# Optimization experiments

Measured on AMD Instinct MI355X. Metric: run time of the kernel, lower is better.

## Reference

```python
import jax, jax.numpy as jnp
import numpy as np

B, S, H = 64, 1024, 1024

def setup_inputs() -> dict:
    key = jax.random.key(0)
    k1, k2, k3, k4, k5 = jax.random.split(key, 5)
    scale = 1.0 / np.sqrt(H)
    return {
        "decoder_state": jax.random.normal(k1, (B, H), dtype=jnp.float32),
        "encoder_outputs": jax.random.normal(k2, (B, S, H), dtype=jnp.float32),
        "mask": jnp.ones((B, S), dtype=jnp.int32),
        "W_s": jax.random.uniform(k3, (H, H), minval=-scale, maxval=scale, dtype=jnp.float32),
        "W_h": jax.random.uniform(k4, (H, H), minval=-scale, maxval=scale, dtype=jnp.float32),
        "v": jax.random.uniform(k5, (H,), minval=-scale, maxval=scale, dtype=jnp.float32),
    }

def reference(decoder_state, encoder_outputs, mask, W_s, W_h, v):
    # Additive (Bahdanau) attention.
    # proj_s: [B, H] -- original applies W_s to the expanded state (same math, computed once)
    proj_s = decoder_state @ W_s.T
    # proj_h: [B, S, H]
    proj_h = jnp.einsum('bsh,kh->bsk', encoder_outputs, W_h)
    energy = jnp.tanh(proj_s[:, None, :] + proj_h)          # [B, S, H]
    scores = jnp.einsum('bsh,h->bs', energy, v)             # [B, S]
    scores = jnp.where(mask == 0, -jnp.inf, scores)
    weights = jax.nn.softmax(scores, axis=-1)               # [B, S]
    context = jnp.einsum('bs,bsh->bh', weights, encoder_outputs)  # [B, H]
    return context, weights
```

## Files before the change

### kernel.cpp

```cpp
#include <hip/hip_runtime.h>
#include <hip/hip_bf16.h>

#define B_ 64
#define S_ 1024
#define H_ 1024
#define M_ (B_*S_)

typedef __attribute__((ext_vector_type(8))) short short8;
typedef __attribute__((ext_vector_type(4))) float f32x4;

__device__ __forceinline__ unsigned short f2bf(float f) {
    union { float f; unsigned u; } c; c.f = f;
    unsigned u = c.u;
    unsigned r = (u + 0x7fffu + ((u >> 16) & 1u)) >> 16;
    return (unsigned short)r;
}

__device__ __forceinline__ float bf2f(unsigned short h) {
    union { unsigned u; float f; } c; c.u = ((unsigned)h) << 16;
    return c.f;
}

__device__ __forceinline__ float tanh_fast(float x) {
    float t = __expf(2.0f * x);
    return 1.0f - 2.0f * __builtin_amdgcn_rcpf(t + 1.0f);
}

__device__ __forceinline__ void gll16(const unsigned short* g, unsigned short* l) {
    auto* gp = (const __attribute__((address_space(1))) unsigned short*)(g);
    auto* lp = (__attribute__((address_space(3))) unsigned short*)(l);
    __builtin_amdgcn_global_load_lds(gp, lp, 16, 0, 0);
}

__global__ void cvt_bf16_kernel(const float* __restrict__ src,
                                unsigned short* __restrict__ dst, int n8) {
    int idx = blockIdx.x * blockDim.x + threadIdx.x;
    int stride = gridDim.x * blockDim.x;
    for (int i = idx; i < n8; i += stride) {
        const float4* s4 = (const float4*)src + (size_t)i * 2;
        float4 a = s4[0], b = s4[1];
        short8 o;
        o[0] = f2bf(a.x); o[1] = f2bf(a.y); o[2] = f2bf(a.z); o[3] = f2bf(a.w);
        o[4] = f2bf(b.x); o[5] = f2bf(b.y); o[6] = f2bf(b.z); o[7] = f2bf(b.w);
        *((short8*)dst + i) = o;
    }
}

__global__ void proj_s_part_kernel(const float* __restrict__ dec,
                                   const float* __restrict__ Ws,
                                   float* __restrict__ part) {
    __shared__ float wss[64][68];
    const int kt = blockIdx.x & 15, hs = blockIdx.x >> 4;
    const int k0 = kt * 64, h0 = hs * 64;
    const int t = threadIdx.x;

    {
        const int r = t >> 2, c = (t & 3) * 16;
        const float4* src = (const float4*)(Ws + (size_t)(k0 + r) * H_ + h0 + c);
        float4 v0 = src[0], v1 = src[1], v2 = src[2], v3 = src[3];
        *(float4*)&wss[r][c + 0]  = v0;
        *(float4*)&wss[r][c + 4]  = v1;
        *(float4*)&wss[r][c + 8]  = v2;
        *(float4*)&wss[r][c + 12] = v3;
    }
    const int b = t >> 2, kq = t & 3;
    float4 dreg[16];
    const float4* dsrc = (const float4*)(dec + (size_t)b * H_ + h0);
#pragma unroll
    for (int i = 0; i < 16; ++i) dreg[i] = dsrc[i];
    __syncthreads();

    float acc[16] = {};
#pragma unroll
    for (int h4 = 0; h4 < 16; ++h4) {
        float4 d = dreg[h4];
#pragma unroll
        for (int j = 0; j < 16; ++j) {
            float4 wv = *(const float4*)&wss[kq + 4 * j][h4 * 4];
            acc[j] = fmaf(d.x, wv.x, acc[j]);
            acc[j] = fmaf(d.y, wv.y, acc[j]);
            acc[j] = fmaf(d.z, wv.z, acc[j]);
            acc[j] = fmaf(d.w, wv.w, acc[j]);
        }
    }
#pragma unroll
    for (int j = 0; j < 16; ++j)
        part[(size_t)hs * M_ + b * H_ + k0 + kq + 4 * j] = acc[j];
}

__global__ void proj_red_kernel(const float* __restrict__ part,
                                float* __restrict__ proj_s) {
    int i = blockIdx.x * 256 + threadIdx.x;
    float s = 0.0f;
#pragma unroll
    for (int p = 0; p < 16; ++p) s += part[(size_t)p * M_ + i];
    proj_s[i] = s;
}

__global__ void fused_scores_bf16_kernel(const unsigned short* __restrict__ encb,
                                         const unsigned short* __restrict__ Whb,
                                         const float* __restrict__ proj_s,
                                         const float* __restrict__ v,
                                         float* __restrict__ scores_part) {
    __shared__ __align__(16) unsigned short AsF[128 * 32];
    __shared__ __align__(16) unsigned short BsF[128 * 32];
    __shared__ float sums[128][2];

    const int bx0 = blockIdx.x;
    const int bx = (bx0 & 7) * 512 + (bx0 >> 3);
    const int nt = bx & 7;
    const int mt = bx >> 3;
    const int t = threadIdx.x;
    const int w = t >> 6, lane = t & 63;
    const int wr = w >> 1, wc = w & 1;
    const int lrow = lane & 15, lgrp = lane >> 4;

    f32x4 acc[4][4] = {};

    const int srow = lane >> 2;
    const int scol = (lane & 3) * 8;
    const unsigned short* gA0 = encb + (size_t)(mt * 128 + w * 32 + srow) * H_ + scol;
    const unsigned short* gA1 = gA0 + 16 * H_;
    const unsigned short* gB0 = Whb + (size_t)(nt * 128 + w * 32 + srow) * H_ + scol;
    const unsigned short* gB1 = gB0 + 16 * H_;
    unsigned short* lA0 = AsF + (w * 2 + 0) * 512;
    unsigned short* lA1 = AsF + (w * 2 + 1) * 512;
    unsigned short* lB0 = BsF + (w * 2 + 0) * 512;
    unsigned short* lB1 = BsF + (w * 2 + 1) * 512;

    for (int kt = 0; kt < H_ / 32; ++kt) {
        __syncthreads();
        gll16(gA0 + kt * 32, lA0);
        gll16(gA1 + kt * 32, lA1);
        gll16(gB0 + kt * 32, lB0);
        gll16(gB1 + kt * 32, lB1);
        __syncthreads();

        short8 af[4], bf[4];
#pragma unroll
        for (int m = 0; m < 4; ++m)
            af[m] = *(const short8*)&AsF[(wr * 64 + m * 16 + lrow) * 32 + lgrp * 8];
#pragma unroll
        for (int n = 0; n < 4; ++n)
            bf[n] = *(const short8*)&BsF[(wc * 64 + n * 16 + lrow) * 32 + lgrp * 8];
#pragma unroll
        for (int m = 0; m < 4; ++m)
#pragma unroll
            for (int n = 0; n < 4; ++n)
                acc[m][n] = __builtin_amdgcn_mfma_f32_16x16x32_bf16(af[m], bf[n], acc[m][n], 0, 0, 0);
    }

    const int b = mt >> 3;
    float vv[4], ps[4];
#pragma unroll
    for (int n = 0; n < 4; ++n) {
        int col = nt * 128 + wc * 64 + n * 16 + lrow;
        vv[n] = v[col];
        ps[n] = proj_s[b * H_ + col];
    }
    float rs[4][4];
#pragma unroll
    for (int m = 0; m < 4; ++m) {
#pragma unroll
        for (int j = 0; j < 4; ++j) {
            float s = 0.0f;
#pragma unroll
            for (int n = 0; n < 4; ++n)
                s = fmaf(tanh_fast(acc[m][n][j] + ps[n]), vv[n], s);
            s += __shfl_xor(s, 1, 64);
            s += __shfl_xor(s, 2, 64);
            s += __shfl_xor(s, 4, 64);
            s += __shfl_xor(s, 8, 64);
            rs[m][j] = s;
        }
    }
    if (lrow == 0) {
#pragma unroll
        for (int m = 0; m < 4; ++m)
#pragma unroll
            for (int j = 0; j < 4; ++j)
                sums[wr * 64 + m * 16 + lgrp * 4 + j][wc] = rs[m][j];
    }
    __syncthreads();
    if (t < 128)
        scores_part[(size_t)nt * M_ + mt * 128 + t] = sums[t][0] + sums[t][1];
}

__global__ void fused_scores_kernel(const float* __restrict__ enc,
                                    const float* __restrict__ Wh,
                                    const float* __restrict__ proj_s,
                                    const float* __restrict__ v,
                                    float* __restrict__ scores_part) {
    __shared__ __align__(16) unsigned short As[128][40];
    __shared__ __align__(16) unsigned short Bs[128][40];
    __shared__ float sums[128][2];

    const int bx = blockIdx.x;
    const int nt = bx & 7;
    const int mt = bx >> 3;
    const int t = threadIdx.x;
    const int w = t >> 6, lane = t & 63;
    const int wr = w >> 1, wc = w & 1;
    const int lrow = lane & 15, lgrp = lane >> 4;

    f32x4 acc[4][4] = {};

    const int srow = t >> 1;
    const int shalf = t & 1;
    const float* gA = enc + (size_t)(mt * 128 + srow) * H_ + shalf * 16;
    const float* gB = Wh  + (size_t)(nt * 128 + srow) * H_ + shalf * 16;
    unsigned short* lA = &As[srow][shalf * 16];
    unsigned short* lB = &Bs[srow][shalf * 16];

    for (int kt = 0; kt < H_ / 32; ++kt) {
        __syncthreads();
        const float4* a4 = (const float4*)(gA + kt * 32);
        const float4* b4 = (const float4*)(gB + kt * 32);
        union { unsigned short us[16]; uint4 q[2]; } pa, pb;
#pragma unroll
        for (int i = 0; i < 4; ++i) {
            float4 av = a4[i];
            float4 bv = b4[i];
            pa.us[i*4+0] = f2bf(av.x); pa.us[i*4+1] = f2bf(av.y);
            pa.us[i*4+2] = f2bf(av.z); pa.us[i*4+3] = f2bf(av.w);
            pb.us[i*4+0] = f2bf(bv.x); pb.us[i*4+1] = f2bf(bv.y);
            pb.us[i*4+2] = f2bf(bv.z); pb.us[i*4+3] = f2bf(bv.w);
        }
        *(uint4*)(lA)     = pa.q[0];
        *(uint4*)(lA + 8) = pa.q[1];
        *(uint4*)(lB)     = pb.q[0];
        *(uint4*)(lB + 8) = pb.q[1];
        __syncthreads();

        short8 af[4], bf[4];
#pragma unroll
        for (int m = 0; m < 4; ++m)
            af[m] = *(const short8*)&As[wr * 64 + m * 16 + lrow][lgrp * 8];
#pragma unroll
        for (int n = 0; n < 4; ++n)
            bf[n] = *(const short8*)&Bs[wc * 64 + n * 16 + lrow][lgrp * 8];
#pragma unroll
        for (int m = 0; m < 4; ++m)
#pragma unroll
            for (int n = 0; n < 4; ++n)
                acc[m][n] = __builtin_amdgcn_mfma_f32_16x16x32_bf16(af[m], bf[n], acc[m][n], 0, 0, 0);
    }

    const int b = mt >> 3;
    float vv[4], ps[4];
#pragma unroll
    for (int n = 0; n < 4; ++n) {
        int col = nt * 128 + wc * 64 + n * 16 + lrow;
        vv[n] = v[col];
        ps[n] = proj_s[b * H_ + col];
    }
    float rs[4][4];
#pragma unroll
    for (int m = 0; m < 4; ++m) {
#pragma unroll
        for (int j = 0; j < 4; ++j) {
            float s = 0.0f;
#pragma unroll
            for (int n = 0; n < 4; ++n)
                s = fmaf(tanh_fast(acc[m][n][j] + ps[n]), vv[n], s);
            s += __shfl_xor(s, 1, 64);
            s += __shfl_xor(s, 2, 64);
            s += __shfl_xor(s, 4, 64);
            s += __shfl_xor(s, 8, 64);
            rs[m][j] = s;
        }
    }
    if (lrow == 0) {
#pragma unroll
        for (int m = 0; m < 4; ++m)
#pragma unroll
            for (int j = 0; j < 4; ++j)
                sums[wr * 64 + m * 16 + lgrp * 4 + j][wc] = rs[m][j];
    }
    __syncthreads();
    if (t < 128)
        scores_part[(size_t)nt * M_ + mt * 128 + t] = sums[t][0] + sums[t][1];
}

__global__ void softmax_kernel(const float* __restrict__ scores_part,
                               const int* __restrict__ mask,
                               float* __restrict__ weights) {
    const int b = blockIdx.x, t = threadIdx.x;
    __shared__ float red[8];
    float sc[4];
#pragma unroll
    for (int i = 0; i < 4; ++i) {
        int s = t + i * 256;
        float x = 0.0f;
#pragma unroll
        for (int p = 0; p < 8; ++p)
            x += scores_part[(size_t)p * M_ + b * S_ + s];
        if (mask[b * S_ + s] == 0) x = -INFINITY;
        sc[i] = x;
    }
    float mx = fmaxf(fmaxf(sc[0], sc[1]), fmaxf(sc[2], sc[3]));
#pragma unroll
    for (int m = 32; m >= 1; m >>= 1) mx = fmaxf(mx, __shfl_xor(mx, m, 64));
    if ((t & 63) == 0) red[t >> 6] = mx;
    __syncthreads();
    mx = fmaxf(fmaxf(red[0], red[1]), fmaxf(red[2], red[3]));

    float e[4]; float sum = 0.0f;
#pragma unroll
    for (int i = 0; i < 4; ++i) { e[i] = __expf(sc[i] - mx); sum += e[i]; }
#pragma unroll
    for (int m = 32; m >= 1; m >>= 1) sum += __shfl_xor(sum, m, 64);
    if ((t & 63) == 0) red[4 + (t >> 6)] = sum;
    __syncthreads();
    sum = red[4] + red[5] + red[6] + red[7];
    float inv = 1.0f / sum;
#pragma unroll
    for (int i = 0; i < 4; ++i)
        weights[b * S_ + t + i * 256] = e[i] * inv;
}

__global__ void context_part_bf16_kernel(const unsigned short* __restrict__ encb,
                                         const float* __restrict__ weights,
                                         float* __restrict__ ctx_part) {
    const int b = blockIdx.x >> 5;
    const int sc = blockIdx.x & 31;
    const int t = threadIdx.x;
    __shared__ float wv[32];
    if (t < 32) wv[t] = weights[b * S_ + sc * 32 + t];
    __syncthreads();
    const short8* e8 = (const short8*)(encb + (size_t)(b * S_ + sc * 32) * H_) + t;
    float a[8] = {};
#pragma unroll 4
    for (int i = 0; i < 32; ++i) {
        short8 ev = e8[(size_t)i * 128];
        float w = wv[i];
#pragma unroll
        for (int j = 0; j < 8; ++j)
            a[j] = fmaf(w, bf2f((unsigned short)ev[j]), a[j]);
    }
    float* dst = ctx_part + (size_t)sc * M_ + b * H_ + t * 8;
    float4 o0; o0.x = a[0]; o0.y = a[1]; o0.z = a[2]; o0.w = a[3];
    float4 o1; o1.x = a[4]; o1.y = a[5]; o1.z = a[6]; o1.w = a[7];
    *(float4*)dst = o0;
    *(float4*)(dst + 4) = o1;
}

__global__ void context_part_kernel(const float* __restrict__ enc,
                                    const float* __restrict__ weights,
                                    float* __restrict__ ctx_part) {
    const int b = blockIdx.x >> 4;
    const int sc = blockIdx.x & 15;
    const int t = threadIdx.x;
    __shared__ float wv[64];
    if (t < 64) wv[t] = weights[b * S_ + sc * 64 + t];
    __syncthreads();
    const float4* e4 = (const float4*)(enc + (size_t)(b * S_ + sc * 64) * H_) + t;
    float ax = 0.f, ay = 0.f, az = 0.f, aw = 0.f;
#pragma unroll 4
    for (int i = 0; i < 64; ++i) {
        float4 ev = e4[i * 256];
        float wgt = wv[i];
        ax = fmaf(wgt, ev.x, ax);
        ay = fmaf(wgt, ev.y, ay);
        az = fmaf(wgt, ev.z, az);
        aw = fmaf(wgt, ev.w, aw);
    }
    float4 o; o.x = ax; o.y = ay; o.z = az; o.w = aw;
    *((float4*)(ctx_part + (size_t)sc * M_ + b * H_) + t) = o;
}

__global__ void ctx_reduce_kernel(const float* __restrict__ ctx_part,
                                  float* __restrict__ ctx, int np) {
    int idx = blockIdx.x * 256 + threadIdx.x;
    float s = 0.0f;
    for (int p = 0; p < np; ++p) s += ctx_part[(size_t)p * M_ + idx];
    ctx[idx] = s;
}

extern "C" void kernel_launch(void* const* d_in, const int* in_sizes, int n_in,
                              void* d_out, int out_size, void* d_ws, size_t ws_size,
                              hipStream_t stream) {
    const float* dec  = (const float*)d_in[0];
    const float* enc  = (const float*)d_in[1];
    const int*   mask = (const int*)d_in[2];
    const float* Ws   = (const float*)d_in[3];
    const float* Wh   = (const float*)d_in[4];
    const float* v    = (const float*)d_in[5];

    float* out = (float*)d_out;

    float* proj_s      = (float*)d_ws;
    float* proj_part   = proj_s + M_;
    float* scores_part = proj_part + 16 * (size_t)M_;
    float* ctx_part    = scores_part + 8 * (size_t)M_;
    unsigned short* encb = (unsigned short*)(ctx_part + 32 * (size_t)M_);
    unsigned short* Whb  = encb + (size_t)B_ * S_ * H_;

    const size_t need_small = 4ull * (1 + 16 + 8 + 32) * M_;
    const size_t need_big   = need_small + 2ull * ((size_t)B_ * S_ * H_ + (size_t)H_ * H_);

    proj_s_part_kernel<<<256, 256, 0, stream>>>(dec, Ws, proj_part);
    proj_red_kernel<<<256, 256, 0, stream>>>(proj_part, proj_s);

    if (ws_size >= need_big) {
        cvt_bf16_kernel<<<2048, 256, 0, stream>>>(enc, encb, B_ * S_ * H_ / 8);
        cvt_bf16_kernel<<<512, 256, 0, stream>>>(Wh, Whb, H_ * H_ / 8);
        fused_scores_bf16_kernel<<<4096, 256, 0, stream>>>(encb, Whb, proj_s, v, scores_part);
        softmax_kernel<<<64, 256, 0, stream>>>(scores_part, mask, out + M_);
        context_part_bf16_kernel<<<2048, 128, 0, stream>>>(encb, out + M_, ctx_part);
        ctx_reduce_kernel<<<256, 256, 0, stream>>>(ctx_part, out, 32);
    } else {
        fused_scores_kernel<<<4096, 256, 0, stream>>>(enc, Wh, proj_s, v, scores_part);
        softmax_kernel<<<64, 256, 0, stream>>>(scores_part, mask, out + M_);
        context_part_kernel<<<1024, 256, 0, stream>>>(enc, out + M_, ctx_part);
        ctx_reduce_kernel<<<256, 256, 0, stream>>>(ctx_part, out, 16);
    }
}
```

Before: 277.4 us.

## Rewrite bf16 scores GEMM as 256x256-tile, 8-wave, double-buffered pipelined kernel

Replaces the 128x128 single-buffered MFMA scores kernel with a 256x256-tile, 512-thread kernel. It double-buffers LDS with direct global-to-LDS loads issued ahead, uses XOR-swizzled LDS layout to avoid bank conflicts, and interleaves MFMA phases with s_setprio and barriers. Larger tiles halve redundant reloads of A/B and reduce partial-score slices from 8 to 4, so softmax now takes a partial count argument. Risks include higher register pressure from 32 accumulators per thread and only 1024 blocks, which lowers occupancy.

Measured after the change: 280.8 us. Within noise of the previous version (+1.2%).

```diff
diff --git a/kernel.cpp b/kernel.cpp
--- a/kernel.cpp
+++ b/kernel.cpp
@@ -97,70 +97,101 @@
     proj_s[i] = s;
 }
 
-__global__ void fused_scores_bf16_kernel(const unsigned short* __restrict__ encb,
-                                         const unsigned short* __restrict__ Whb,
-                                         const float* __restrict__ proj_s,
-                                         const float* __restrict__ v,
-                                         float* __restrict__ scores_part) {
-    __shared__ __align__(16) unsigned short AsF[128 * 32];
-    __shared__ __align__(16) unsigned short BsF[128 * 32];
-    __shared__ float sums[128][2];
+__global__ void __launch_bounds__(512)
+fused_scores_8p_kernel(const unsigned short* __restrict__ encb,
+                       const unsigned short* __restrict__ Whb,
+                       const float* __restrict__ proj_s,
+                       const float* __restrict__ v,
+                       float* __restrict__ scores_part) {
+    __shared__ __align__(16) unsigned short Lsh[32768];
 
     const int bx0 = blockIdx.x;
-    const int bx = (bx0 & 7) * 512 + (bx0 >> 3);
-    const int nt = bx & 7;
-    const int mt = bx >> 3;
+    const int bx = (bx0 & 7) * 128 + (bx0 >> 3);
+    const int nt = bx & 3;
+    const int mt = bx >> 2;
     const int t = threadIdx.x;
-    const int w = t >> 6, lane = t & 63;
-    const int wr = w >> 1, wc = w & 1;
+    const int wid = t >> 6, lane = t & 63;
+    const int wr = wid >> 2, wc = wid & 3;
     const int lrow = lane & 15, lgrp = lane >> 4;
 
-    f32x4 acc[4][4] = {};
-
-    const int srow = lane >> 2;
-    const int scol = (lane & 3) * 8;
-    const unsigned short* gA0 = encb + (size_t)(mt * 128 + w * 32 + srow) * H_ + scol;
-    const unsigned short* gA1 = gA0 + 16 * H_;
-    const unsigned short* gB0 = Whb + (size_t)(nt * 128 + w * 32 + srow) * H_ + scol;
-    const unsigned short* gB1 = gB0 + 16 * H_;
-    unsigned short* lA0 = AsF + (w * 2 + 0) * 512;
-    unsigned short* lA1 = AsF + (w * 2 + 1) * 512;
-    unsigned short* lB0 = BsF + (w * 2 + 0) * 512;
-    unsigned short* lB1 = BsF + (w * 2 + 1) * 512;
-
-    for (int kt = 0; kt < H_ / 32; ++kt) {
-        __syncthreads();
-        gll16(gA0 + kt * 32, lA0);
-        gll16(gA1 + kt * 32, lA1);
-        gll16(gB0 + kt * 32, lB0);
-        gll16(gB1 + kt * 32, lB1);
-        __syncthreads();
-
-        short8 af[4], bf[4];
-#pragma unroll
-        for (int m = 0; m < 4; ++m)
-            af[m] = *(const short8*)&AsF[(wr * 64 + m * 16 + lrow) * 32 + lgrp * 8];
-#pragma unroll
-        for (int n = 0; n < 4; ++n)
-            bf[n] = *(const short8*)&BsF[(wc * 64 + n * 16 + lrow) * 32 + lgrp * 8];
-#pragma unroll
-        for (int m = 0; m < 4; ++m)
-#pragma unroll
-            for (int n = 0; n < 4; ++n)
-                acc[m][n] = __builtin_amdgcn_mfma_f32_16x16x32_bf16(af[m], bf[n], acc[m][n], 0, 0, 0);
-    }
-
-    const int b = mt >> 3;
+    f32x4 acc[8][4] = {};
+
+    const int srow = t >> 2;
+    const int scol = ((t & 3) ^ ((t >> 3) & 3)) * 8;
+    const unsigned short* gA = encb + (size_t)(mt * 256 + srow) * H_ + scol;
+    const unsigned short* gB = Whb  + (size_t)(nt * 256 + srow) * H_ + scol;
+    unsigned short* lws = Lsh + wid * 512;
+
+    #define STAGE(c, op, h, kt) \
+        gll16(((op) ? gB : gA) + (size_t)(h) * (128 * H_) + (kt) * 32, \
+              lws + (c) * 16384 + (op) * 8192 + (h) * 4096)
+
+    int aoff[8], boff[4];
+#pragma unroll
+    for (int m = 0; m < 8; ++m) {
+        int row = wr * 128 + m * 16 + lrow;
+        aoff[m] = row * 64 + ((lgrp ^ ((row >> 1) & 3)) * 16);
+    }
+#pragma unroll
+    for (int n = 0; n < 4; ++n) {
+        int row = wc * 64 + n * 16 + lrow;
+        boff[n] = row * 64 + ((lgrp ^ ((row >> 1) & 3)) * 16);
+    }
+
+    STAGE(0, 0, 0, 0); STAGE(0, 0, 1, 0); STAGE(0, 1, 0, 0); STAGE(0, 1, 1, 0);
+    STAGE(1, 0, 0, 1); STAGE(1, 0, 1, 1); STAGE(1, 1, 0, 1);
+    asm volatile("s_waitcnt vmcnt(3)" ::: "memory");
+    __builtin_amdgcn_sched_barrier(0);
+    __builtin_amdgcn_s_barrier();
+
+    int cur = 0;
+    for (int kt = 0; kt < 32; ++kt) {
+#pragma unroll
+        for (int p = 0; p < 4; ++p) {
+            const int qm = p >> 1, qn = p & 1;
+            short8 af[4], bfr[2];
+#pragma unroll
+            for (int mm = 0; mm < 4; ++mm)
+                af[mm] = *(const short8*)((const char*)Lsh + cur * 32768 + aoff[qm * 4 + mm]);
+#pragma unroll
+            for (int nn = 0; nn < 2; ++nn)
+                bfr[nn] = *(const short8*)((const char*)Lsh + cur * 32768 + 16384 + boff[qn * 2 + nn]);
+            if (p == 0 && kt + 1 < 32) { STAGE(cur ^ 1, 1, 1, kt + 1); }
+            __builtin_amdgcn_s_barrier();
+            __builtin_amdgcn_s_setprio(1);
+#pragma unroll
+            for (int mm = 0; mm < 4; ++mm)
+#pragma unroll
+                for (int nn = 0; nn < 2; ++nn)
+                    acc[qm * 4 + mm][qn * 2 + nn] =
+                        __builtin_amdgcn_mfma_f32_16x16x32_bf16(af[mm], bfr[nn],
+                            acc[qm * 4 + mm][qn * 2 + nn], 0, 0, 0);
+            __builtin_amdgcn_s_setprio(0);
+            __builtin_amdgcn_s_barrier();
+        }
+        if (kt + 2 < 32) {
+            STAGE(cur, 0, 0, kt + 2);
+            STAGE(cur, 0, 1, kt + 2);
+            STAGE(cur, 1, 0, kt + 2);
+        }
+        asm volatile("s_waitcnt vmcnt(3)" ::: "memory");
+        __builtin_amdgcn_sched_barrier(0);
+        __builtin_amdgcn_s_barrier();
+        cur ^= 1;
+    }
+    #undef STAGE
+
+    const int b = mt >> 2;
     float vv[4], ps[4];
 #pragma unroll
     for (int n = 0; n < 4; ++n) {
-        int col = nt * 128 + wc * 64 + n * 16 + lrow;
+        int col = nt * 256 + wc * 64 + n * 16 + lrow;
         vv[n] = v[col];
         ps[n] = proj_s[b * H_ + col];
     }
-    float rs[4][4];
-#pragma unroll
-    for (int m = 0; m < 4; ++m) {
+    float* sums = (float*)Lsh;
+#pragma unroll
+    for (int m = 0; m < 8; ++m) {
 #pragma unroll
         for (int j = 0; j < 4; ++j) {
             float s = 0.0f;
@@ -171,19 +202,15 @@
             s += __shfl_xor(s, 2, 64);
             s += __shfl_xor(s, 4, 64);
             s += __shfl_xor(s, 8, 64);
-            rs[m][j] = s;
-        }
-    }
-    if (lrow == 0) {
-#pragma unroll
-        for (int m = 0; m < 4; ++m)
-#pragma unroll
-            for (int j = 0; j < 4; ++j)
-                sums[wr * 64 + m * 16 + lgrp * 4 + j][wc] = rs[m][j];
-    }
-    __syncthreads();
-    if (t < 128)
-        scores_part[(size_t)nt * M_ + mt * 128 + t] = sums[t][0] + sums[t][1];
+            if (lrow == 0)
+                sums[(wr * 128 + m * 16 + lgrp * 4 + j) * 4 + wc] = s;
+        }
+    }
+    __syncthreads();
+    if (t < 256) {
+        float r = sums[t * 4 + 0] + sums[t * 4 + 1] + sums[t * 4 + 2] + sums[t * 4 + 3];
+        scores_part[(size_t)nt * M_ + mt * 256 + t] = r;
+    }
 }
 
 __global__ void fused_scores_kernel(const float* __restrict__ enc,
@@ -284,7 +311,7 @@
 
 __global__ void softmax_kernel(const float* __restrict__ scores_part,
                                const int* __restrict__ mask,
-                               float* __restrict__ weights) {
+                               float* __restrict__ weights, int np) {
     const int b = blockIdx.x, t = threadIdx.x;
     __shared__ float red[8];
     float sc[4];
@@ -292,8 +319,7 @@
     for (int i = 0; i < 4; ++i) {
         int s = t + i * 256;
         float x = 0.0f;
-#pragma unroll
-        for (int p = 0; p < 8; ++p)
+        for (int p = 0; p < np; ++p)
             x += scores_part[(size_t)p * M_ + b * S_ + s];
         if (mask[b * S_ + s] == 0) x = -INFINITY;
         sc[i] = x;
@@ -405,13 +431,13 @@
     if (ws_size >= need_big) {
         cvt_bf16_kernel<<<2048, 256, 0, stream>>>(enc, encb, B_ * S_ * H_ / 8);
         cvt_bf16_kernel<<<512, 256, 0, stream>>>(Wh, Whb, H_ * H_ / 8);
-        fused_scores_bf16_kernel<<<4096, 256, 0, stream>>>(encb, Whb, proj_s, v, scores_part);
-        softmax_kernel<<<64, 256, 0, stream>>>(scores_part, mask, out + M_);
+        fused_scores_8p_kernel<<<1024, 512, 0, stream>>>(encb, Whb, proj_s, v, scores_part);
+        softmax_kernel<<<64, 256, 0, stream>>>(scores_part, mask, out + M_, 4);
         context_part_bf16_kernel<<<2048, 128, 0, stream>>>(encb, out + M_, ctx_part);
         ctx_reduce_kernel<<<256, 256, 0, stream>>>(ctx_part, out, 32);
     } else {
         fused_scores_kernel<<<4096, 256, 0, stream>>>(enc, Wh, proj_s, v, scores_part);
-        softmax_kernel<<<64, 256, 0, stream>>>(scores_part, mask, out + M_);
+        softmax_kernel<<<64, 256, 0, stream>>>(scores_part, mask, out + M_, 8);
         context_part_kernel<<<1024, 256, 0, stream>>>(enc, out + M_, ctx_part);
         ctx_reduce_kernel<<<256, 256, 0, stream>>>(ctx_part, out, 16);
     }
```
